# Optimization experiments

Measured on AMD Instinct MI355X. Metric: run time of the kernel, lower is better.

## Reference

```python
import jax, jax.numpy as jnp
import numpy as np

N = 100_000
E = 1_600_000
C_IN, C_HID, C_OUT = 128, 128, 64


def setup_inputs() -> dict:
    key = jax.random.key(0)
    ks = jax.random.split(key, 10)
    inp = {
        "x": jax.random.normal(ks[0], (N, C_IN), dtype=jnp.float32),
        "edge_index": jax.random.randint(ks[1], (2, E), 0, N, dtype=jnp.int64),
        "edge_weight": jax.random.uniform(ks[2], (E,), dtype=jnp.float32),
        # learned params: 2 hidden GCN layers + output GCN layer (glorot-ish scale)
        "W1": jax.random.normal(ks[3], (C_IN, C_HID), dtype=jnp.float32) / np.sqrt(C_IN),
        "b1": jnp.zeros((C_HID,), dtype=jnp.float32),
        "W2": jax.random.normal(ks[4], (C_HID, C_HID), dtype=jnp.float32) / np.sqrt(C_HID),
        "b2": jnp.zeros((C_HID,), dtype=jnp.float32),
        "W3": jax.random.normal(ks[5], (C_HID, C_OUT), dtype=jnp.float32) / np.sqrt(C_HID),
        "b3": jnp.zeros((C_OUT,), dtype=jnp.float32),
    }
    return inp


def _gcn_conv(x, src, dst, w, W, b):
    # PyG GCNConv: h = X @ W; out[j] = sum_{(i->j)} norm_ij * h[i] + b
    # norm_ij = deg_i^{-1/2} * w_ij * deg_j^{-1/2}, deg = weighted in-degree (incl. self loops)
    h = x @ W                                      # [N, out]
    deg = jax.ops.segment_sum(w, dst, num_segments=N)  # [N]
    dinv = jnp.where(deg > 0, jax.lax.rsqrt(deg), 0.0)
    norm = dinv[src] * w * dinv[dst]               # [E']
    msg = h[src] * norm[:, None]                   # [E', out] gather-scale
    out = jax.ops.segment_sum(msg, dst, num_segments=N)  # scatter-add
    return out + b


def reference(x, edge_index, edge_weight, W1, b1, W2, b2, W3, b3):
    # add self loops once (weight 1.0), as GCNConv does per layer
    loop = jnp.arange(N, dtype=edge_index.dtype)
    src = jnp.concatenate([edge_index[0], loop])
    dst = jnp.concatenate([edge_index[1], loop])
    w = jnp.concatenate([edge_weight, jnp.ones((N,), dtype=edge_weight.dtype)])

    h = _gcn_conv(x, src, dst, w, W1, b1)
    h = jax.nn.relu(h)          # Dropout is identity in eval mode
    h = _gcn_conv(h, src, dst, w, W2, b2)
    h = jax.nn.relu(h)
    out = _gcn_conv(h, src, dst, w, W3, b3)
    return out
```

## Files before the change

### kernel.cpp

```cpp
#include <hip/hip_runtime.h>
#include <cstdint>
#include <cstddef>

#define TPB 256
#define PKS 16

__device__ __forceinline__ unsigned short f2bf(float f) {
  unsigned u = __float_as_uint(f);
  u += 0x7fffu + ((u >> 16) & 1u);
  return (unsigned short)(u >> 16);
}
__device__ __forceinline__ float bf_lo(unsigned u) { return __uint_as_float(u << 16); }
__device__ __forceinline__ float bf_hi(unsigned u) { return __uint_as_float(u & 0xffff0000u); }

#define FIXP32 8192.0f
#define DEGMASK 0xFFFFFu

typedef __attribute__((ext_vector_type(8))) short  short8v;
typedef __attribute__((ext_vector_type(4))) float  float4v;


__global__ void init_k(unsigned* __restrict__ pk, int n) {
  int i = blockIdx.x * TPB + threadIdx.x;
  if (i < n * PKS) pk[i] = 0u;
}

__global__ void edges_k(const int* __restrict__ ei, const float* __restrict__ w,
                        unsigned* __restrict__ pk, int* __restrict__ pir, int E) {
  int e = blockIdx.x * TPB + threadIdx.x;
  if (e >= E) return;
  int d = ei[E + e];
  unsigned v = (1u << 20) | (unsigned)(w[e] * FIXP32 + 0.5f);
  unsigned old = atomicAdd(&pk[(size_t)d * PKS], v);
  pir[e] = (int)(old >> 20);
}

__global__ void unpack_k(const unsigned* __restrict__ pk,
                         float* __restrict__ dinv, int* __restrict__ cnt, int n) {
  int i = blockIdx.x * TPB + threadIdx.x;
  if (i >= n) return;
  unsigned p = pk[(size_t)i * PKS];
  float deg = 1.0f + (float)(p & DEGMASK) * (1.0f / FIXP32);
  dinv[i] = rsqrtf(deg);
  cnt[i]  = (int)(p >> 20);
}

__global__ void scan_a(const int* __restrict__ cnt, int* __restrict__ rp,
                       int* __restrict__ bsum, int n) {
  __shared__ int s[TPB];
  int i = blockIdx.x * TPB + threadIdx.x;
  int v = (i < n) ? cnt[i] : 0;
  s[threadIdx.x] = v;
  __syncthreads();
  #pragma unroll
  for (int off = 1; off < TPB; off <<= 1) {
    int t = (threadIdx.x >= off) ? s[threadIdx.x - off] : 0;
    __syncthreads();
    s[threadIdx.x] += t;
    __syncthreads();
  }
  if (i < n) rp[i] = s[threadIdx.x] - v;
  if (threadIdx.x == TPB - 1) bsum[blockIdx.x] = s[TPB - 1];
}

__global__ void scan_b(int* __restrict__ bsum, int nb) {
  __shared__ int s[512];
  int v = (threadIdx.x < nb) ? bsum[threadIdx.x] : 0;
  s[threadIdx.x] = v;
  __syncthreads();
  #pragma unroll
  for (int off = 1; off < 512; off <<= 1) {
    int t = (threadIdx.x >= off) ? s[threadIdx.x - off] : 0;
    __syncthreads();
    s[threadIdx.x] += t;
    __syncthreads();
  }
  if (threadIdx.x < nb) bsum[threadIdx.x] = s[threadIdx.x] - v;
}

__global__ void scan_c(int* __restrict__ rp, const int* __restrict__ bsum, int n, int etot) {
  int i = blockIdx.x * TPB + threadIdx.x;
  if (i < n) rp[i] += bsum[blockIdx.x];
  if (blockIdx.x == 0 && threadIdx.x == 0) rp[n] = etot;
}

__global__ void fill_k(const int* __restrict__ ei, const float* __restrict__ w,
                       const float* __restrict__ dinv, const int* __restrict__ rp,
                       const int* __restrict__ pir, int2* __restrict__ epk, int E) {
  int e = blockIdx.x * TPB + threadIdx.x;
  if (e >= E) return;
  int s = ei[e];
  int d = ei[E + e];
  int pos = rp[d] + pir[e];
  float nrm = dinv[s] * w[e] * dinv[d];
  epk[pos] = make_int2(s, __float_as_int(nrm));
}

__global__ void wt_k(const float* __restrict__ W1, const float* __restrict__ W2,
                     const float* __restrict__ W3,
                     unsigned short* __restrict__ wt1, unsigned short* __restrict__ wt2,
                     unsigned short* __restrict__ wt3) {
  int t = blockIdx.x * TPB + threadIdx.x;
  if (t < 16384) {
    int c = t >> 7, k = t & 127;
    wt1[t] = f2bf(W1[k * 128 + c]);
  } else if (t < 32768) {
    int u = t - 16384;
    int c = u >> 7, k = u & 127;
    wt2[u] = f2bf(W2[k * 128 + c]);
  } else if (t < 40960) {
    int u = t - 32768;
    int c = u >> 7, k = u & 127;
    wt3[u] = f2bf(W3[k * 64 + c]);
  }
}


template<int COUT, bool RELU, bool BF16IN>
__global__ __launch_bounds__(256) void gemm_mfma(const void* __restrict__ Xv,
                                                 const unsigned short* __restrict__ Wt,
                                                 unsigned short* __restrict__ H, int n) {
  const int lane = threadIdx.x & 63;
  const int wv   = threadIdx.x >> 6;
  const int r0   = (blockIdx.x * 4 + wv) * 16;
  if (r0 >= n) return;
  const int c16   = lane & 15;
  const int kb    = (lane >> 4) * 8;
  const int row_c = min(r0 + c16, n - 1);

  short8v a[4];
  if (BF16IN) {
    const unsigned short* xrow = (const unsigned short*)Xv + (size_t)row_c * 128;
    #pragma unroll
    for (int kk = 0; kk < 4; kk++) {
      short8v t = *(const short8v*)(xrow + kk * 32 + kb);
      if (RELU) {
        #pragma unroll
        for (int j = 0; j < 8; j++) t[j] = (short)(t[j] & 0x8000) ? (short)0 : t[j];
      }
      a[kk] = t;
    }
  } else {
    const float* xrow = (const float*)Xv + (size_t)row_c * 128;
    #pragma unroll
    for (int kk = 0; kk < 4; kk++) {
      float4 lo = *(const float4*)(xrow + kk * 32 + kb);
      float4 hi = *(const float4*)(xrow + kk * 32 + kb + 4);
      float v0 = lo.x, v1 = lo.y, v2 = lo.z, v3 = lo.w;
      float v4 = hi.x, v5 = hi.y, v6 = hi.z, v7 = hi.w;
      if (RELU) {
        v0 = fmaxf(v0, 0.f); v1 = fmaxf(v1, 0.f); v2 = fmaxf(v2, 0.f); v3 = fmaxf(v3, 0.f);
        v4 = fmaxf(v4, 0.f); v5 = fmaxf(v5, 0.f); v6 = fmaxf(v6, 0.f); v7 = fmaxf(v7, 0.f);
      }
      short8v t;
      t[0] = (short)f2bf(v0); t[1] = (short)f2bf(v1);
      t[2] = (short)f2bf(v2); t[3] = (short)f2bf(v3);
      t[4] = (short)f2bf(v4); t[5] = (short)f2bf(v5);
      t[6] = (short)f2bf(v6); t[7] = (short)f2bf(v7);
      a[kk] = t;
    }
  }

  constexpr int CT = COUT / 16;
  const int orow = r0 + (lane >> 4) * 4;
  #pragma unroll
  for (int ct = 0; ct < CT; ct++) {
    float4v acc = {0.f, 0.f, 0.f, 0.f};
    const unsigned short* wrow = Wt + (size_t)(ct * 16 + c16) * 128 + kb;
    #pragma unroll
    for (int kk = 0; kk < 4; kk++) {
      short8v b = *(const short8v*)(wrow + kk * 32);
      acc = __builtin_amdgcn_mfma_f32_16x16x32_bf16(a[kk], b, acc, 0, 0, 0);
    }
    const int ocol = ct * 16 + c16;
    #pragma unroll
    for (int r = 0; r < 4; r++) {
      if (orow + r < n)
        H[(size_t)(orow + r) * COUT + ocol] = f2bf(acc[r]);
    }
  }
}


__global__ __launch_bounds__(256) void agg128(const unsigned short* __restrict__ H,
                                              const int* __restrict__ rp,
                                              const int2* __restrict__ epk,
                                              const float* __restrict__ dinv,
                                              const float* __restrict__ bias,
                                              unsigned* __restrict__ OUT, int n) {
  int wid  = __builtin_amdgcn_readfirstlane(blockIdx.x * 4 + (threadIdx.x >> 6));
  int lane = threadIdx.x & 63;
  if (wid >= n) return;
  float di = dinv[wid];
  float w0 = di * di;
  unsigned hv = ((const unsigned*)(H + (size_t)wid * 128))[lane];
  float2 bv = ((const float2*)bias)[lane];
  float ax = bv.x + w0 * bf_lo(hv);
  float ay = bv.y + w0 * bf_hi(hv);
  int e  = rp[wid];
  int e1 = rp[wid + 1];
  for (; e + 15 < e1; e += 16) {
    int2 p[16];
    #pragma unroll
    for (int u = 0; u < 16; u++) p[u] = epk[e + u];
    unsigned h[16];
    #pragma unroll
    for (int u = 0; u < 16; u++) h[u] = ((const unsigned*)(H + (size_t)p[u].x * 128))[lane];
    #pragma unroll
    for (int u = 0; u < 16; u++) {
      float nw = __int_as_float(p[u].y);
      ax += nw * bf_lo(h[u]);
      ay += nw * bf_hi(h[u]);
    }
  }
  for (; e + 3 < e1; e += 4) {
    int2 p[4];
    #pragma unroll
    for (int u = 0; u < 4; u++) p[u] = epk[e + u];
    unsigned h[4];
    #pragma unroll
    for (int u = 0; u < 4; u++) h[u] = ((const unsigned*)(H + (size_t)p[u].x * 128))[lane];
    #pragma unroll
    for (int u = 0; u < 4; u++) {
      float nw = __int_as_float(p[u].y);
      ax += nw * bf_lo(h[u]);
      ay += nw * bf_hi(h[u]);
    }
  }
  for (; e < e1; e++) {
    int2 p = epk[e];
    unsigned h = ((const unsigned*)(H + (size_t)p.x * 128))[lane];
    float nw = __int_as_float(p.y);
    ax += nw * bf_lo(h); ay += nw * bf_hi(h);
  }
  OUT[(size_t)wid * 64 + lane] = (unsigned)f2bf(ax) | ((unsigned)f2bf(ay) << 16);
}

__global__ __launch_bounds__(256) void agg64(const unsigned short* __restrict__ H,
                                             const int* __restrict__ rp,
                                             const int2* __restrict__ epk,
                                             const float* __restrict__ dinv,
                                             const float* __restrict__ bias,
                                             float* __restrict__ OUT, int n) {
  int wid  = __builtin_amdgcn_readfirstlane(blockIdx.x * 4 + (threadIdx.x >> 6));
  int lane = threadIdx.x & 63;
  if (wid >= n) return;
  float di = dinv[wid];
  float w0 = di * di;
  float hv = __uint_as_float(((unsigned)H[(size_t)wid * 64 + lane]) << 16);
  float acc = bias[lane] + w0 * hv;
  int e  = rp[wid];
  int e1 = rp[wid + 1];
  for (; e + 15 < e1; e += 16) {
    int2 p[16];
    #pragma unroll
    for (int u = 0; u < 16; u++) p[u] = epk[e + u];
    float h[16];
    #pragma unroll
    for (int u = 0; u < 16; u++)
      h[u] = __uint_as_float(((unsigned)H[(size_t)p[u].x * 64 + lane]) << 16);
    #pragma unroll
    for (int u = 0; u < 16; u++) acc += __int_as_float(p[u].y) * h[u];
  }
  for (; e + 3 < e1; e += 4) {
    int2 p[4];
    #pragma unroll
    for (int u = 0; u < 4; u++) p[u] = epk[e + u];
    float h[4];
    #pragma unroll
    for (int u = 0; u < 4; u++)
      h[u] = __uint_as_float(((unsigned)H[(size_t)p[u].x * 64 + lane]) << 16);
    #pragma unroll
    for (int u = 0; u < 4; u++) acc += __int_as_float(p[u].y) * h[u];
  }
  for (; e < e1; e++) {
    int2 p = epk[e];
    float h = __uint_as_float(((unsigned)H[(size_t)p.x * 64 + lane]) << 16);
    acc += __int_as_float(p.y) * h;
  }
  OUT[(size_t)wid * 64 + lane] = acc;
}


extern "C" void kernel_launch(void* const* d_in, const int* in_sizes, int n_in,
                              void* d_out, int out_size, void* d_ws, size_t ws_size,
                              hipStream_t stream) {
  const float* x  = (const float*)d_in[0];
  const int*   ei = (const int*)d_in[1];
  const float* ew = (const float*)d_in[2];
  const float* W1 = (const float*)d_in[3];
  const float* b1 = (const float*)d_in[4];
  const float* W2 = (const float*)d_in[5];
  const float* b2 = (const float*)d_in[6];
  const float* W3 = (const float*)d_in[7];
  const float* b3 = (const float*)d_in[8];

  const int N = in_sizes[0] / 128;
  const int E = in_sizes[2];

  char* p = (char*)d_ws;
  auto carve = [&](size_t bytes) -> void* {
    void* r = (void*)p;
    p += (bytes + 255) & ~(size_t)255;
    return r;
  };
  unsigned* pk  = (unsigned*)carve((size_t)N * 4 * PKS);
  float* dinv   = (float*)carve((size_t)N * 4);
  int*   cnt    = (int*)  carve((size_t)N * 4);
  int*   rp     = (int*)  carve((size_t)(N + 1) * 4);
  int*   bsum   = (int*)  carve(512 * 4);
  int*   pir    = (int*)  carve((size_t)E * 4);
  int2*  epk    = (int2*) carve((size_t)E * 8);
  unsigned short* hbuf = (unsigned short*)carve((size_t)N * 128 * 2);
  unsigned* abuf = (unsigned*)carve((size_t)N * 128 * 2);
  unsigned short* wt1 = (unsigned short*)carve(16384 * 2);
  unsigned short* wt2 = (unsigned short*)carve(16384 * 2);
  unsigned short* wt3 = (unsigned short*)carve(8192 * 2);

  const int NB = (N + TPB - 1) / TPB;
  const int EB = (E + TPB - 1) / TPB;

  init_k<<<(N * PKS + TPB - 1) / TPB, TPB, 0, stream>>>(pk, N);
  edges_k<<<EB, TPB, 0, stream>>>(ei, ew, pk, pir, E);
  unpack_k<<<NB, TPB, 0, stream>>>(pk, dinv, cnt, N);
  scan_a<<<NB, TPB, 0, stream>>>(cnt, rp, bsum, N);
  scan_b<<<1, 512, 0, stream>>>(bsum, NB);
  scan_c<<<NB, TPB, 0, stream>>>(rp, bsum, N, E);
  fill_k<<<EB, TPB, 0, stream>>>(ei, ew, dinv, rp, pir, epk, E);
  wt_k<<<160, TPB, 0, stream>>>(W1, W2, W3, wt1, wt2, wt3);

  const int aggBlocks  = (N + 3) / 4;
  const int gemmBlocks = (N + 63) / 64;

  gemm_mfma<128, false, false><<<gemmBlocks, 256, 0, stream>>>(x, wt1, hbuf, N);
  agg128<<<aggBlocks, 256, 0, stream>>>(hbuf, rp, epk, dinv, b1, abuf, N);

  gemm_mfma<128, true, true><<<gemmBlocks, 256, 0, stream>>>(abuf, wt2, hbuf, N);
  agg128<<<aggBlocks, 256, 0, stream>>>(hbuf, rp, epk, dinv, b2, abuf, N);

  gemm_mfma<64, true, true><<<gemmBlocks, 256, 0, stream>>>(abuf, wt3, hbuf, N);
  agg64<<<aggBlocks, 256, 0, stream>>>(hbuf, rp, epk, dinv, b3, (float*)d_out, N);
}
```

Measured before the change: 363.1 us.

## Fuse edge degree atomics with first GEMM and drop padded degree counters

Launches the edge-degree atomic pass and the first-layer MFMA GEMM as one kernel, split by block index, so the atomic-bound edge work overlaps with the compute-bound GEMM. The per-node counters are no longer padded to 16 words, and a memset replaces the init kernel, which shrinks the zeroing traffic. The unpadded counters put neighbouring nodes' atomics on shared cache lines, which may add contention. The weight-transpose kernel moves earlier so its output is ready before the fused kernel runs.

```diff
diff --git a/kernel.cpp b/kernel.cpp
--- a/kernel.cpp
+++ b/kernel.cpp
@@ -3,7 +3,6 @@
 #include <cstddef>
 
 #define TPB 256
-#define PKS 16
 
 __device__ __forceinline__ unsigned short f2bf(float f) {
   unsigned u = __float_as_uint(f);
@@ -20,26 +19,94 @@
 typedef __attribute__((ext_vector_type(4))) float  float4v;
 
 
-__global__ void init_k(unsigned* __restrict__ pk, int n) {
-  int i = blockIdx.x * TPB + threadIdx.x;
-  if (i < n * PKS) pk[i] = 0u;
-}
-
-__global__ void edges_k(const int* __restrict__ ei, const float* __restrict__ w,
-                        unsigned* __restrict__ pk, int* __restrict__ pir, int E) {
-  int e = blockIdx.x * TPB + threadIdx.x;
-  if (e >= E) return;
-  int d = ei[E + e];
-  unsigned v = (1u << 20) | (unsigned)(w[e] * FIXP32 + 0.5f);
-  unsigned old = atomicAdd(&pk[(size_t)d * PKS], v);
-  pir[e] = (int)(old >> 20);
+template<int COUT, bool RELU, bool BF16IN>
+__device__ __forceinline__ void gemm_body(int bid, const void* __restrict__ Xv,
+                                          const unsigned short* __restrict__ Wt,
+                                          unsigned short* __restrict__ H, int n) {
+  const int lane = threadIdx.x & 63;
+  const int wv   = threadIdx.x >> 6;
+  const int r0   = (bid * 4 + wv) * 16;
+  if (r0 >= n) return;
+  const int c16   = lane & 15;
+  const int kb    = (lane >> 4) * 8;
+  const int row_c = min(r0 + c16, n - 1);
+
+  short8v a[4];
+  if (BF16IN) {
+    const unsigned short* xrow = (const unsigned short*)Xv + (size_t)row_c * 128;
+    #pragma unroll
+    for (int kk = 0; kk < 4; kk++) {
+      short8v t = *(const short8v*)(xrow + kk * 32 + kb);
+      if (RELU) {
+        #pragma unroll
+        for (int j = 0; j < 8; j++) t[j] = (short)(t[j] & 0x8000) ? (short)0 : t[j];
+      }
+      a[kk] = t;
+    }
+  } else {
+    const float* xrow = (const float*)Xv + (size_t)row_c * 128;
+    #pragma unroll
+    for (int kk = 0; kk < 4; kk++) {
+      float4 lo = *(const float4*)(xrow + kk * 32 + kb);
+      float4 hi = *(const float4*)(xrow + kk * 32 + kb + 4);
+      float v0 = lo.x, v1 = lo.y, v2 = lo.z, v3 = lo.w;
+      float v4 = hi.x, v5 = hi.y, v6 = hi.z, v7 = hi.w;
+      if (RELU) {
+        v0 = fmaxf(v0, 0.f); v1 = fmaxf(v1, 0.f); v2 = fmaxf(v2, 0.f); v3 = fmaxf(v3, 0.f);
+        v4 = fmaxf(v4, 0.f); v5 = fmaxf(v5, 0.f); v6 = fmaxf(v6, 0.f); v7 = fmaxf(v7, 0.f);
+      }
+      short8v t;
+      t[0] = (short)f2bf(v0); t[1] = (short)f2bf(v1);
+      t[2] = (short)f2bf(v2); t[3] = (short)f2bf(v3);
+      t[4] = (short)f2bf(v4); t[5] = (short)f2bf(v5);
+      t[6] = (short)f2bf(v6); t[7] = (short)f2bf(v7);
+      a[kk] = t;
+    }
+  }
+
+  constexpr int CT = COUT / 16;
+  const int orow = r0 + (lane >> 4) * 4;
+  #pragma unroll
+  for (int ct = 0; ct < CT; ct++) {
+    float4v acc = {0.f, 0.f, 0.f, 0.f};
+    const unsigned short* wrow = Wt + (size_t)(ct * 16 + c16) * 128 + kb;
+    #pragma unroll
+    for (int kk = 0; kk < 4; kk++) {
+      short8v b = *(const short8v*)(wrow + kk * 32);
+      acc = __builtin_amdgcn_mfma_f32_16x16x32_bf16(a[kk], b, acc, 0, 0, 0);
+    }
+    const int ocol = ct * 16 + c16;
+    #pragma unroll
+    for (int r = 0; r < 4; r++) {
+      if (orow + r < n)
+        H[(size_t)(orow + r) * COUT + ocol] = f2bf(acc[r]);
+    }
+  }
+}
+
+
+__global__ __launch_bounds__(256) void fused_edges_gemm1(
+    const int* __restrict__ ei, const float* __restrict__ w,
+    unsigned* __restrict__ pk, int* __restrict__ pir, int E, int eb,
+    const float* __restrict__ X, const unsigned short* __restrict__ Wt,
+    unsigned short* __restrict__ H, int n) {
+  if (blockIdx.x < (unsigned)eb) {
+    int e = blockIdx.x * TPB + threadIdx.x;
+    if (e >= E) return;
+    int d = ei[E + e];
+    unsigned v = (1u << 20) | (unsigned)(w[e] * FIXP32 + 0.5f);
+    unsigned old = atomicAdd(&pk[d], v);
+    pir[e] = (int)(old >> 20);
+  } else {
+    gemm_body<128, false, false>(blockIdx.x - eb, X, Wt, H, n);
+  }
 }
 
 __global__ void unpack_k(const unsigned* __restrict__ pk,
                          float* __restrict__ dinv, int* __restrict__ cnt, int n) {
   int i = blockIdx.x * TPB + threadIdx.x;
   if (i >= n) return;
-  unsigned p = pk[(size_t)i * PKS];
+  unsigned p = pk[i];
   float deg = 1.0f + (float)(p & DEGMASK) * (1.0f / FIXP32);
   dinv[i] = rsqrtf(deg);
   cnt[i]  = (int)(p >> 20);
@@ -115,70 +182,11 @@
   }
 }
 
-
 template<int COUT, bool RELU, bool BF16IN>
 __global__ __launch_bounds__(256) void gemm_mfma(const void* __restrict__ Xv,
                                                  const unsigned short* __restrict__ Wt,
                                                  unsigned short* __restrict__ H, int n) {
-  const int lane = threadIdx.x & 63;
-  const int wv   = threadIdx.x >> 6;
-  const int r0   = (blockIdx.x * 4 + wv) * 16;
-  if (r0 >= n) return;
-  const int c16   = lane & 15;
-  const int kb    = (lane >> 4) * 8;
-  const int row_c = min(r0 + c16, n - 1);
-
-  short8v a[4];
-  if (BF16IN) {
-    const unsigned short* xrow = (const unsigned short*)Xv + (size_t)row_c * 128;
-    #pragma unroll
-    for (int kk = 0; kk < 4; kk++) {
-      short8v t = *(const short8v*)(xrow + kk * 32 + kb);
-      if (RELU) {
-        #pragma unroll
-        for (int j = 0; j < 8; j++) t[j] = (short)(t[j] & 0x8000) ? (short)0 : t[j];
-      }
-      a[kk] = t;
-    }
-  } else {
-    const float* xrow = (const float*)Xv + (size_t)row_c * 128;
-    #pragma unroll
-    for (int kk = 0; kk < 4; kk++) {
-      float4 lo = *(const float4*)(xrow + kk * 32 + kb);
-      float4 hi = *(const float4*)(xrow + kk * 32 + kb + 4);
-      float v0 = lo.x, v1 = lo.y, v2 = lo.z, v3 = lo.w;
-      float v4 = hi.x, v5 = hi.y, v6 = hi.z, v7 = hi.w;
-      if (RELU) {
-        v0 = fmaxf(v0, 0.f); v1 = fmaxf(v1, 0.f); v2 = fmaxf(v2, 0.f); v3 = fmaxf(v3, 0.f);
-        v4 = fmaxf(v4, 0.f); v5 = fmaxf(v5, 0.f); v6 = fmaxf(v6, 0.f); v7 = fmaxf(v7, 0.f);
-      }
-      short8v t;
-      t[0] = (short)f2bf(v0); t[1] = (short)f2bf(v1);
-      t[2] = (short)f2bf(v2); t[3] = (short)f2bf(v3);
-      t[4] = (short)f2bf(v4); t[5] = (short)f2bf(v5);
-      t[6] = (short)f2bf(v6); t[7] = (short)f2bf(v7);
-      a[kk] = t;
-    }
-  }
-
-  constexpr int CT = COUT / 16;
-  const int orow = r0 + (lane >> 4) * 4;
-  #pragma unroll
-  for (int ct = 0; ct < CT; ct++) {
-    float4v acc = {0.f, 0.f, 0.f, 0.f};
-    const unsigned short* wrow = Wt + (size_t)(ct * 16 + c16) * 128 + kb;
-    #pragma unroll
-    for (int kk = 0; kk < 4; kk++) {
-      short8v b = *(const short8v*)(wrow + kk * 32);
-      acc = __builtin_amdgcn_mfma_f32_16x16x32_bf16(a[kk], b, acc, 0, 0, 0);
-    }
-    const int ocol = ct * 16 + c16;
-    #pragma unroll
-    for (int r = 0; r < 4; r++) {
-      if (orow + r < n)
-        H[(size_t)(orow + r) * COUT + ocol] = f2bf(acc[r]);
-    }
-  }
+  gemm_body<COUT, RELU, BF16IN>(blockIdx.x, Xv, Wt, H, n);
 }
 
 
@@ -304,7 +312,7 @@
     p += (bytes + 255) & ~(size_t)255;
     return r;
   };
-  unsigned* pk  = (unsigned*)carve((size_t)N * 4 * PKS);
+  unsigned* pk  = (unsigned*)carve((size_t)N * 4);
   float* dinv   = (float*)carve((size_t)N * 4);
   int*   cnt    = (int*)  carve((size_t)N * 4);
   int*   rp     = (int*)  carve((size_t)(N + 1) * 4);
@@ -319,20 +327,19 @@
 
   const int NB = (N + TPB - 1) / TPB;
   const int EB = (E + TPB - 1) / TPB;
-
-  init_k<<<(N * PKS + TPB - 1) / TPB, TPB, 0, stream>>>(pk, N);
-  edges_k<<<EB, TPB, 0, stream>>>(ei, ew, pk, pir, E);
+  const int aggBlocks  = (N + 3) / 4;
+  const int gemmBlocks = (N + 63) / 64;
+
+  hipMemsetAsync(pk, 0, (size_t)N * 4, stream);
+  wt_k<<<160, TPB, 0, stream>>>(W1, W2, W3, wt1, wt2, wt3);
+  fused_edges_gemm1<<<EB + gemmBlocks, TPB, 0, stream>>>(
+      ei, ew, pk, pir, E, EB, x, wt1, hbuf, N);
   unpack_k<<<NB, TPB, 0, stream>>>(pk, dinv, cnt, N);
   scan_a<<<NB, TPB, 0, stream>>>(cnt, rp, bsum, N);
   scan_b<<<1, 512, 0, stream>>>(bsum, NB);
   scan_c<<<NB, TPB, 0, stream>>>(rp, bsum, N, E);
   fill_k<<<EB, TPB, 0, stream>>>(ei, ew, dinv, rp, pir, epk, E);
-  wt_k<<<160, TPB, 0, stream>>>(W1, W2, W3, wt1, wt2, wt3);
-
-  const int aggBlocks  = (N + 3) / 4;
-  const int gemmBlocks = (N + 63) / 64;
-
-  gemm_mfma<128, false, false><<<gemmBlocks, 256, 0, stream>>>(x, wt1, hbuf, N);
+
   agg128<<<aggBlocks, 256, 0, stream>>>(hbuf, rp, epk, dinv, b1, abuf, N);
 
   gemm_mfma<128, true, true><<<gemmBlocks, 256, 0, stream>>>(abuf, wt2, hbuf, N);
```

Measured after the change: 365.0 us. Within noise of the previous version (+0.5%).
